# Optimization experiments

Hardware: AMD Instinct MI355X
Metric: run time of the kernel (lower is better)

## Reference

```python
import jax, jax.numpy as jnp
import numpy as np
import math

B, N, D, O, H = 2, 3072, 64, 64, 4

def setup_inputs() -> dict:
    key = jax.random.key(0)
    ks = jax.random.split(key, 8)
    x = jax.random.normal(ks[0], (B, N, D), dtype=jnp.float32)
    edge_index = jax.random.randint(ks[1], (B, N, N), 0, 2, dtype=jnp.int32)
    s = 1.0 / math.sqrt(D)
    Wv = jax.random.uniform(ks[2], (H, D, O), jnp.float32, -s, s)
    bv = jax.random.uniform(ks[3], (H, O), jnp.float32, -s, s)
    Wq = jax.random.uniform(ks[4], (H, D, O), jnp.float32, -s, s)
    bq = jax.random.uniform(ks[5], (H, O), jnp.float32, -s, s)
    Wk = jax.random.uniform(ks[6], (H, D, O), jnp.float32, -s, s)
    bk = jax.random.uniform(ks[7], (H, O), jnp.float32, -s, s)
    return {"x": x, "edge_index": edge_index, "Wv": Wv, "bv": bv,
            "Wq": Wq, "bq": bq, "Wk": Wk, "bk": bk}

def reference(x, edge_index, Wv, bv, Wq, bq, Wk, bk):
    # x: [B,N,D]; edge_index: dense {0,1} adjacency [B,N,N]
    dk = jnp.asarray(math.sqrt(x.shape[-1]), x.dtype)
    v = jnp.einsum('bnd,hdo->bhno', x, Wv) + bv[None, :, None, :]
    q = jnp.einsum('bnd,hdo->bhno', x, Wq) + bq[None, :, None, :]
    k = jnp.einsum('bnd,hdo->bhno', x, Wk) + bk[None, :, None, :]
    scores = jnp.einsum('bhno,bhmo->bhnm', q, k) / dk        # [B,H,N,N]
    scores = jax.nn.leaky_relu(scores, 0.2)
    mask = (-1e10) * (1.0 - edge_index.astype(scores.dtype))  # [B,N,N]
    scores = scores + mask[:, None, :, :]
    prop = jax.nn.softmax(scores, axis=-1)
    # dropout on v omitted (inference mode: identity)
    feats = jnp.einsum('bhnm,bhmo->bhno', prop, v)            # [B,H,N,O]
    out = jnp.mean(feats, axis=1)                             # [B,N,O]
    return jax.nn.leaky_relu(out, 0.2)
```

## Files before the change

### kernel.cpp

```cpp
#include <hip/hip_runtime.h>
#include <hip/hip_bf16.h>
#include <cstdint>

#define Bc 2
#define Nc 3072
#define Hc 4
#define NW32 96
#define TILEB 8192

typedef __bf16    bf16x8 __attribute__((ext_vector_type(8)));
typedef _Float16  f16x8  __attribute__((ext_vector_type(8)));
typedef float     f32x16 __attribute__((ext_vector_type(16)));

#define QSCALE 0.18033688f

static __device__ __forceinline__ f32x16 mfma32bf(bf16x8 a, bf16x8 b, f32x16 c) {
    return __builtin_amdgcn_mfma_f32_32x32x16_bf16(a, b, c, 0, 0, 0);
}
static __device__ __forceinline__ f32x16 mfma32h(f16x8 a, f16x8 b, f32x16 c) {
    return __builtin_amdgcn_mfma_f32_32x32x16_f16(a, b, c, 0, 0, 0);
}
static __device__ __forceinline__ void gload_lds16(const void* g, void* l) {
    __builtin_amdgcn_global_load_lds((const __attribute__((address_space(1))) void*)g,
                                     (__attribute__((address_space(3))) void*)l, 16, 0, 0);
}
static __device__ __forceinline__ uint32_t pkrtz(float lo, float hi) {
    uint32_t w;
    asm("v_cvt_pkrtz_f16_f32 %0, %1, %2" : "=v"(w) : "v"(lo), "v"(hi));
    return w;
}

static __device__ __forceinline__ void softmax_pack(const f32x16& sc, uint32_t mwh,
                                                    uint32_t W8[8], float& lsum)
{
    #pragma unroll
    for (int i = 0; i < 8; ++i) {
        const int bp0 = (2*i & 3) + 8*(2*i >> 2);
        float s0 = sc[2*i], s1 = sc[2*i + 1];
        float a0 = fmaxf(s0, 0.2f*s0);
        float a1 = fmaxf(s1, 0.2f*s1);
        float e0, e1;
        asm("v_exp_f32 %0, %1" : "=v"(e0) : "v"(a0));
        asm("v_exp_f32 %0, %1" : "=v"(e1) : "v"(a1));
        uint32_t m0 = (uint32_t)(((int)(mwh << (31 - bp0))) >> 31);
        uint32_t m1 = (uint32_t)(((int)(mwh << (30 - bp0))) >> 31);
        float p0 = __uint_as_float(__float_as_uint(e0) & m0);
        float p1 = __uint_as_float(__float_as_uint(e1) & m1);
        lsum += p0 + p1;
        W8[i] = pkrtz(p0, p1);
    }
}

static __device__ __forceinline__ void assemble_pa(uint32_t W8[8], f16x8& pa0, f16x8& pa1)
{
    uint32_t a0 = W8[0], a2 = W8[2], a1 = W8[1], a3 = W8[3];
    uint32_t b0 = W8[4], b2 = W8[6], b1 = W8[5], b3 = W8[7];
    asm("v_permlane32_swap_b32 %0, %1" : "+v"(a0), "+v"(a2));
    asm("v_permlane32_swap_b32 %0, %1" : "+v"(a1), "+v"(a3));
    asm("v_permlane32_swap_b32 %0, %1" : "+v"(b0), "+v"(b2));
    asm("v_permlane32_swap_b32 %0, %1" : "+v"(b1), "+v"(b3));
    union { uint32_t u[4]; f16x8 v; } u0, u1;
    u0.u[0] = a0; u0.u[1] = a1; u0.u[2] = a2; u0.u[3] = a3;
    u1.u[0] = b0; u1.u[1] = b1; u1.u[2] = b2; u1.u[3] = b3;
    pa0 = u0.v; pa1 = u1.v;
}

__global__ void prep_kernel(const float* __restrict__ Wq, const float* __restrict__ Wk,
                            const float* __restrict__ Wv,
                            const float* __restrict__ bq, const float* __restrict__ bk,
                            const float* __restrict__ bv, const float* __restrict__ x,
                            __bf16* __restrict__ Wbh, __bf16* __restrict__ Wbl,
                            float* __restrict__ Bs,
                            __bf16* __restrict__ Xh, __bf16* __restrict__ Xl)
{
    if (blockIdx.x < 192) {
        int i = blockIdx.x*256 + threadIdx.x;
        int d = i & 63, o = (i >> 6) & 63, h = (i >> 12) & 3, p = i >> 14;
        const float* W = (p == 0) ? Wq : (p == 1) ? Wk : Wv;
        float scale = (p == 0) ? QSCALE : 1.0f;
        float val = W[(h*64 + d)*64 + o] * scale;
        int idx = (((p*Hc + h)*64 + o) << 6) + d;
        __bf16 hi = (__bf16)val;
        Wbh[idx] = hi;
        Wbl[idx] = (__bf16)(val - (float)hi);
        if (i < 3*Hc*64) {
            int pp = i / (Hc*64), rest = i % (Hc*64);
            const float* B = (pp == 0) ? bq : (pp == 1) ? bk : bv;
            Bs[i] = B[rest] * ((pp == 0) ? QSCALE : 1.0f);
        }
    } else {
        int i = (blockIdx.x - 192)*256 + threadIdx.x;
        const float4* xp = (const float4*)(x + (size_t)i*8);
        float4 a = xp[0], c = xp[1];
        float v[8] = {a.x, a.y, a.z, a.w, c.x, c.y, c.z, c.w};
        bf16x8 h, l;
        #pragma unroll
        for (int j = 0; j < 8; ++j) {
            __bf16 hh = (__bf16)v[j];
            h[j] = hh;
            l[j] = (__bf16)(v[j] - (float)hh);
        }
        *(bf16x8*)(Xh + (size_t)i*8) = h;
        *(bf16x8*)(Xl + (size_t)i*8) = l;
    }
}

__global__ __launch_bounds__(256) void qkv_mfma(
    const __bf16* __restrict__ Xh, const __bf16* __restrict__ Xl,
    const __bf16* __restrict__ Wbh, const __bf16* __restrict__ Wbl,
    const float* __restrict__ Bs,
    _Float16* __restrict__ Qf, _Float16* __restrict__ Kf,
    _Float16* __restrict__ KVimg)
{
    const int lane = threadIdx.x & 63, w = threadIdx.x >> 6;
    const int l31 = lane & 31, hi = lane >> 5;
    int t = blockIdx.x;
    int nt = t % 48; t /= 48;
    int b  = t & 1;  t >>= 1;
    int p  = t % 3;
    int h  = t / 3;
    const int r0 = (w >> 1)*32, c0 = (w & 1)*32, n0 = nt*64;

    bf16x8 xh[4], xl[4], wh[4], wl[4];
    #pragma unroll
    for (int kk = 0; kk < 4; ++kk) {
        size_t xoff = (((size_t)(b*Nc + n0 + r0 + l31)) << 6) + kk*16 + hi*8;
        xh[kk] = *(const bf16x8*)(Xh + xoff);
        xl[kk] = *(const bf16x8*)(Xl + xoff);
        size_t woff = (((size_t)((p*Hc + h)*64 + c0 + l31)) << 6) + kk*16 + hi*8;
        wh[kk] = *(const bf16x8*)(Wbh + woff);
        wl[kk] = *(const bf16x8*)(Wbl + woff);
    }
    float bias = Bs[(p*Hc + h)*64 + c0 + l31];
    f32x16 acc;
    #pragma unroll
    for (int i = 0; i < 16; ++i) acc[i] = bias;
    #pragma unroll
    for (int kk = 0; kk < 4; ++kk) {
        acc = mfma32bf(xh[kk], wh[kk], acc);
        acc = mfma32bf(xl[kk], wh[kk], acc);
        acc = mfma32bf(xh[kk], wl[kk], acc);
    }
    const int bh = b*Hc + h;
    if (p < 2) {
        _Float16* dst = (p == 0) ? Qf : Kf;
        #pragma unroll
        for (int r = 0; r < 16; ++r) {
            int row = (r & 3) + 8*(r >> 2) + 4*hi;
            size_t idx = (((size_t)bh*Nc + n0 + r0 + row) << 6) + c0 + l31;
            dst[idx] = (_Float16)acc[r];
        }
    } else {
        const int t_img = (n0 + r0) >> 5;
        char* img = (char*)KVimg + (size_t)(bh*96 + t_img)*TILEB;
        #pragma unroll
        for (int grp = 0; grp < 2; ++grp) {
            uint32_t wH[4];
            #pragma unroll
            for (int j = 0; j < 4; ++j)
                wH[j] = pkrtz(acc[grp*8 + 2*j], acc[grp*8 + 2*j + 1]);
            asm("v_permlane32_swap_b32 %0, %1" : "+v"(wH[0]), "+v"(wH[2]));
            asm("v_permlane32_swap_b32 %0, %1" : "+v"(wH[1]), "+v"(wH[3]));
            const int kb = grp*2 + hi;
            const int o  = c0 + l31;
            uint4 gh = {wH[0], wH[1], wH[2], wH[3]};
            *(uint4*)(img + 4096 + ((kb*64 + o) << 4)) = gh;
        }
    }
}

__global__ void imgk_kernel(const _Float16* __restrict__ Kf, _Float16* __restrict__ KVimg)
{
    const int t = blockIdx.x % 96, bh = blockIdx.x / 96;
    char* img = (char*)KVimg + (size_t)(bh*96 + t)*TILEB;
    int dc = threadIdx.x & 7, key = threadIdx.x >> 3;
    size_t src = (((size_t)bh*Nc + t*32 + key) << 6) + dc*8;
    *(uint4*)(img + (dc*32 + key)*16) = *(const uint4*)(Kf + src);
}

__global__ void pack_kernel(const int* __restrict__ edge, uint32_t* __restrict__ pmT)
{
    int gw = blockIdx.x*4 + (threadIdx.x >> 6);
    int lane = threadIdx.x & 63;
    int ng = gw % 48; gw /= 48;
    int w  = gw % NW32; gw /= NW32;
    int b  = gw;
    int n = ng*64 + lane;
    const uint4* ep = (const uint4*)(edge + ((size_t)b*Nc + n)*Nc + w*32);
    uint32_t word = 0;
    #pragma unroll
    for (int i = 0; i < 8; ++i) {
        uint4 e = ep[i];
        word |= (e.x ? 1u : 0u) << (4*i);
        word |= (e.y ? 1u : 0u) << (4*i + 1);
        word |= (e.z ? 1u : 0u) << (4*i + 2);
        word |= (e.w ? 1u : 0u) << (4*i + 3);
    }
    pmT[((size_t)b*NW32 + w)*Nc + n] = word;
}

__global__ __launch_bounds__(256, 3) void attn_mfma(
    const _Float16* __restrict__ Qf,
    const _Float16* __restrict__ KVimg, const uint32_t* __restrict__ pmT,
    float* __restrict__ PA, float* __restrict__ PL, int KS, int tps)
{
    __shared__ __align__(16) char lds[3][2*TILEB];
    const int lane = threadIdx.x & 63, w = threadIdx.x >> 6;
    const int l31 = lane & 31, hi = lane >> 5;
    int gb = blockIdx.x;
    const int bh = gb & 7; gb >>= 3;
    const int qt = gb % 24;
    const int ks = gb / 24;
    const int b = bh >> 2;
    const int qrow0 = qt*128 + w*32;
    const int t0 = ks*tps;
    const int iters = tps >> 1;

    const uint32_t* pmp = pmT + ((size_t)b*NW32 + t0)*Nc + qrow0 + l31;
    uint32_t mw0 = pmp[0];
    uint32_t mw1 = pmp[Nc];
    __builtin_amdgcn_sched_barrier(0);
    const char* gsrc = (const char*)KVimg + (size_t)(bh*96 + t0)*TILEB
                     + w*4096 + lane*16;
    #pragma unroll
    for (int g = 0; g < 4; ++g)
        gload_lds16(gsrc + g*1024, &lds[0][w*4096 + g*1024]);

    f16x8 qf[4];
    #pragma unroll
    for (int kk = 0; kk < 4; ++kk) {
        size_t qoff = (((size_t)bh*Nc + qrow0 + l31) << 6) + kk*16 + hi*8;
        qf[kk] = *(const f16x8*)(Qf + qoff);
    }

    f32x16 acc0, acc1;
    #pragma unroll
    for (int i = 0; i < 16; ++i) { acc0[i] = 0.f; acc1[i] = 0.f; }
    float lsum = 0.f;

    char *bA = &lds[0][0], *bB = &lds[1][0], *bC = &lds[2][0];
    #pragma unroll 1
    for (int it = 0; it < iters; ++it) {
        const int adv = (it + 1 < iters) ? 1 : 0;
        const size_t moff = (size_t)(adv ? 2 : 0) * Nc;
        uint32_t nmw0 = pmp[moff];
        uint32_t nmw1 = pmp[moff + Nc];
        pmp += moff;
        __builtin_amdgcn_sched_barrier(0);
        const char* gnext = gsrc + (adv ? 2*TILEB : 0);
        {
            char* ldst = bB + w*4096;
            #pragma unroll
            for (int g = 0; g < 4; ++g)
                gload_lds16(gnext + g*1024, ldst + g*1024);
        }
        gsrc = gnext;
        asm volatile("s_waitcnt vmcnt(6)" ::: "memory");
        __builtin_amdgcn_s_barrier();

        f32x16 sc0, sc1;
        #pragma unroll
        for (int i = 0; i < 16; ++i) { sc0[i] = 0.f; sc1[i] = 0.f; }
        __builtin_amdgcn_s_setprio(1);
        #pragma unroll
        for (int kk = 0; kk < 4; ++kk) {
            f16x8 k0 = *(const f16x8*)(bA + ((kk*2 + hi) << 9) + (l31 << 4));
            f16x8 k1 = *(const f16x8*)(bA + TILEB + ((kk*2 + hi) << 9) + (l31 << 4));
            sc0 = mfma32h(k0, qf[kk], sc0);
            sc1 = mfma32h(k1, qf[kk], sc1);
        }
        __builtin_amdgcn_s_setprio(0);

        uint32_t W80[8], W81[8];
        softmax_pack(sc0, mw0 >> (hi*4), W80, lsum);
        softmax_pack(sc1, mw1 >> (hi*4), W81, lsum);
        mw0 = nmw0; mw1 = nmw1;
        f16x8 pa00, pa01, pa10, pa11;
        assemble_pa(W80, pa00, pa01);
        assemble_pa(W81, pa10, pa11);

        __builtin_amdgcn_s_setprio(1);
        #pragma unroll
        for (int u = 0; u < 2; ++u) {
            #pragma unroll
            for (int kkp = 0; kkp < 2; ++kkp) {
                f16x8 pa = u ? (kkp ? pa11 : pa10) : (kkp ? pa01 : pa00);
                #pragma unroll
                for (int ot = 0; ot < 2; ++ot) {
                    f16x8 vh = *(const f16x8*)(bA + u*TILEB + 4096
                                               + ((kkp*2 + hi) << 10)
                                               + ((ot*32 + l31) << 4));
                    if (ot == 0) acc0 = mfma32h(pa, vh, acc0);
                    else         acc1 = mfma32h(pa, vh, acc1);
                }
            }
        }
        __builtin_amdgcn_s_setprio(0);

        char* tmp = bA; bA = bB; bB = bC; bC = tmp;
    }

    float* po = PA + (((size_t)(bh*KS + ks)*Nc + qrow0) << 6);
    #pragma unroll
    for (int r = 0; r < 16; ++r) {
        int row = (r & 3) + 8*(r >> 2) + 4*hi;
        po[((size_t)row << 6) + l31]      = acc0[r];
        po[((size_t)row << 6) + 32 + l31] = acc1[r];
    }
    lsum += __shfl_xor(lsum, 32);
    if (lane < 32)
        PL[(size_t)(bh*KS + ks)*Nc + qrow0 + l31] = lsum;
}

__global__ void merge_kernel(const float* __restrict__ PA, const float* __restrict__ PL,
                             float* __restrict__ out, int KS)
{
    int gid = blockIdx.x*256 + threadIdx.x;
    int o  = gid & 63;
    int bn = gid >> 6;
    int n  = bn % Nc;
    int b  = bn / Nc;
    float ft = 0.f;
    for (int h = 0; h < Hc; ++h) {
        int bh = b*Hc + h;
        float A = 0.f, L = 0.f;
        for (int ks = 0; ks < KS; ++ks) {
            A += PA[(((size_t)(bh*KS + ks)*Nc + n) << 6) + o];
            L += PL[(size_t)(bh*KS + ks)*Nc + n];
        }
        ft += A / L;
    }
    ft *= 0.25f;
    out[((size_t)bn << 6) + o] = fmaxf(ft, 0.f) + 0.2f*fminf(ft, 0.f);
}

extern "C" void kernel_launch(void* const* d_in, const int* in_sizes, int n_in,
                              void* d_out, int out_size, void* d_ws, size_t ws_size,
                              hipStream_t stream)
{
    const float* x    = (const float*)d_in[0];
    const int*   edge = (const int*)d_in[1];
    const float* Wv   = (const float*)d_in[2];
    const float* bv   = (const float*)d_in[3];
    const float* Wq   = (const float*)d_in[4];
    const float* bq   = (const float*)d_in[5];
    const float* Wk   = (const float*)d_in[6];
    const float* bk   = (const float*)d_in[7];
    float* out = (float*)d_out;

    const size_t PROJ = (size_t)Bc*Hc*Nc*64;
    char* p = (char*)d_ws;
    __bf16* Wbh = (__bf16*)p;     p += 49152*2;
    __bf16* Wbl = (__bf16*)p;     p += 49152*2;
    float*  Bs  = (float*)p;      p += 4096;
    __bf16* Xh  = (__bf16*)p;     p += (size_t)Bc*Nc*64*2;
    __bf16* Xl  = (__bf16*)p;     p += (size_t)Bc*Nc*64*2;
    _Float16* Qf = (_Float16*)p;  p += PROJ*2;
    _Float16* Kf = (_Float16*)p;  p += PROJ*2;
    _Float16* KVimg = (_Float16*)p; p += (size_t)Bc*Hc*96*TILEB;
    uint32_t* pmT = (uint32_t*)p; p += (size_t)Bc*NW32*Nc*4;

    int KS = 4;
    for (;;) {
        size_t need = (size_t)(p - (char*)d_ws)
                    + (size_t)Bc*Hc*KS*Nc*64*4 + (size_t)Bc*Hc*KS*Nc*4;
        if (need <= ws_size || KS == 1) break;
        KS >>= 1;
    }
    float* PA = (float*)p;        p += (size_t)Bc*Hc*KS*Nc*64*4;
    float* PL = (float*)p;

    hipLaunchKernelGGL(prep_kernel, dim3(384),  dim3(256), 0, stream,
                       Wq, Wk, Wv, bq, bk, bv, x, Wbh, Wbl, Bs, Xh, Xl);
    hipLaunchKernelGGL(qkv_mfma,    dim3(1152), dim3(256), 0, stream,
                       Xh, Xl, Wbh, Wbl, Bs, Qf, Kf, KVimg);
    hipLaunchKernelGGL(imgk_kernel, dim3(Bc*Hc*96), dim3(256), 0, stream, Kf, KVimg);
    hipLaunchKernelGGL(pack_kernel, dim3(Bc*NW32*48/4), dim3(256), 0, stream, edge, pmT);
    hipLaunchKernelGGL(attn_mfma,   dim3(8*KS*24), dim3(256), 0, stream,
                       Qf, KVimg, pmT, PA, PL, KS, 96/KS);
    hipLaunchKernelGGL(merge_kernel, dim3((Bc*Nc*64)/256), dim3(256), 0, stream,
                       PA, PL, out, KS);
}
```

Baseline: 80.93 us.

## Split attention K tiles across wave pairs, MFMA row sums, fuse x split into qkv

The attention kernel now runs 512 threads per block. Two waves share each 32-row query slab and take alternating K tiles, and their partial accumulators are combined through LDS at the end. The softmax denominator is now computed by an MFMA against a ones vector instead of scalar adds, and masking is applied to the packed f16 values. The bf16 hi/lo split of x moves from the prep kernel into qkv_mfma, which drops the Xh/Xl workspace round trip, and the split count is fixed at compile time. Risks include register pressure under the (512,6) launch bounds, the extra LDS reduction, and a small precision change in the row sum.

```diff
diff --git a/kernel.cpp b/kernel.cpp
--- a/kernel.cpp
+++ b/kernel.cpp
@@ -7,6 +7,8 @@
 #define Hc 4
 #define NW32 96
 #define TILEB 8192
+#define KSC 4
+#define TPS (NW32/KSC)
 
 typedef __bf16    bf16x8 __attribute__((ext_vector_type(8)));
 typedef _Float16  f16x8  __attribute__((ext_vector_type(8)));
@@ -31,7 +33,7 @@
 }
 
 static __device__ __forceinline__ void softmax_pack(const f32x16& sc, uint32_t mwh,
-                                                    uint32_t W8[8], float& lsum)
+                                                    uint32_t W8[8])
 {
     #pragma unroll
     for (int i = 0; i < 8; ++i) {
@@ -42,12 +44,10 @@
         float e0, e1;
         asm("v_exp_f32 %0, %1" : "=v"(e0) : "v"(a0));
         asm("v_exp_f32 %0, %1" : "=v"(e1) : "v"(a1));
+        uint32_t pk = pkrtz(e0, e1);
         uint32_t m0 = (uint32_t)(((int)(mwh << (31 - bp0))) >> 31);
         uint32_t m1 = (uint32_t)(((int)(mwh << (30 - bp0))) >> 31);
-        float p0 = __uint_as_float(__float_as_uint(e0) & m0);
-        float p1 = __uint_as_float(__float_as_uint(e1) & m1);
-        lsum += p0 + p1;
-        W8[i] = pkrtz(p0, p1);
+        W8[i] = pk & ((m0 & 0x0000ffffu) | (m1 & 0xffff0000u));
     }
 }
 
@@ -68,45 +68,28 @@
 __global__ void prep_kernel(const float* __restrict__ Wq, const float* __restrict__ Wk,
                             const float* __restrict__ Wv,
                             const float* __restrict__ bq, const float* __restrict__ bk,
-                            const float* __restrict__ bv, const float* __restrict__ x,
+                            const float* __restrict__ bv,
                             __bf16* __restrict__ Wbh, __bf16* __restrict__ Wbl,
-                            float* __restrict__ Bs,
-                            __bf16* __restrict__ Xh, __bf16* __restrict__ Xl)
-{
-    if (blockIdx.x < 192) {
-        int i = blockIdx.x*256 + threadIdx.x;
-        int d = i & 63, o = (i >> 6) & 63, h = (i >> 12) & 3, p = i >> 14;
-        const float* W = (p == 0) ? Wq : (p == 1) ? Wk : Wv;
-        float scale = (p == 0) ? QSCALE : 1.0f;
-        float val = W[(h*64 + d)*64 + o] * scale;
-        int idx = (((p*Hc + h)*64 + o) << 6) + d;
-        __bf16 hi = (__bf16)val;
-        Wbh[idx] = hi;
-        Wbl[idx] = (__bf16)(val - (float)hi);
-        if (i < 3*Hc*64) {
-            int pp = i / (Hc*64), rest = i % (Hc*64);
-            const float* B = (pp == 0) ? bq : (pp == 1) ? bk : bv;
-            Bs[i] = B[rest] * ((pp == 0) ? QSCALE : 1.0f);
-        }
-    } else {
-        int i = (blockIdx.x - 192)*256 + threadIdx.x;
-        const float4* xp = (const float4*)(x + (size_t)i*8);
-        float4 a = xp[0], c = xp[1];
-        float v[8] = {a.x, a.y, a.z, a.w, c.x, c.y, c.z, c.w};
-        bf16x8 h, l;
-        #pragma unroll
-        for (int j = 0; j < 8; ++j) {
-            __bf16 hh = (__bf16)v[j];
-            h[j] = hh;
-            l[j] = (__bf16)(v[j] - (float)hh);
-        }
-        *(bf16x8*)(Xh + (size_t)i*8) = h;
-        *(bf16x8*)(Xl + (size_t)i*8) = l;
+                            float* __restrict__ Bs)
+{
+    int i = blockIdx.x*256 + threadIdx.x;
+    int d = i & 63, o = (i >> 6) & 63, h = (i >> 12) & 3, p = i >> 14;
+    const float* W = (p == 0) ? Wq : (p == 1) ? Wk : Wv;
+    float scale = (p == 0) ? QSCALE : 1.0f;
+    float val = W[(h*64 + d)*64 + o] * scale;
+    int idx = (((p*Hc + h)*64 + o) << 6) + d;
+    __bf16 hi = (__bf16)val;
+    Wbh[idx] = hi;
+    Wbl[idx] = (__bf16)(val - (float)hi);
+    if (i < 3*Hc*64) {
+        int pp = i / (Hc*64), rest = i % (Hc*64);
+        const float* B = (pp == 0) ? bq : (pp == 1) ? bk : bv;
+        Bs[i] = B[rest] * ((pp == 0) ? QSCALE : 1.0f);
     }
 }
 
 __global__ __launch_bounds__(256) void qkv_mfma(
-    const __bf16* __restrict__ Xh, const __bf16* __restrict__ Xl,
+    const float* __restrict__ x,
     const __bf16* __restrict__ Wbh, const __bf16* __restrict__ Wbl,
     const float* __restrict__ Bs,
     _Float16* __restrict__ Qf, _Float16* __restrict__ Kf,
@@ -125,8 +108,15 @@
     #pragma unroll
     for (int kk = 0; kk < 4; ++kk) {
         size_t xoff = (((size_t)(b*Nc + n0 + r0 + l31)) << 6) + kk*16 + hi*8;
-        xh[kk] = *(const bf16x8*)(Xh + xoff);
-        xl[kk] = *(const bf16x8*)(Xl + xoff);
+        float4 f0 = *(const float4*)(x + xoff);
+        float4 f1 = *(const float4*)(x + xoff + 4);
+        float xs[8] = {f0.x, f0.y, f0.z, f0.w, f1.x, f1.y, f1.z, f1.w};
+        #pragma unroll
+        for (int j = 0; j < 8; ++j) {
+            __bf16 hh = (__bf16)xs[j];
+            xh[kk][j] = hh;
+            xl[kk][j] = (__bf16)(xs[j] - (float)hh);
+        }
         size_t woff = (((size_t)((p*Hc + h)*64 + c0 + l31)) << 6) + kk*16 + hi*8;
         wh[kk] = *(const bf16x8*)(Wbh + woff);
         wl[kk] = *(const bf16x8*)(Wbl + woff);
@@ -199,32 +189,32 @@
     pmT[((size_t)b*NW32 + w)*Nc + n] = word;
 }
 
-__global__ __launch_bounds__(256, 3) void attn_mfma(
+__global__ __launch_bounds__(512, 6) void attn_mfma(
     const _Float16* __restrict__ Qf,
     const _Float16* __restrict__ KVimg, const uint32_t* __restrict__ pmT,
-    float* __restrict__ PA, float* __restrict__ PL, int KS, int tps)
+    float* __restrict__ PA, float* __restrict__ PL)
 {
     __shared__ __align__(16) char lds[3][2*TILEB];
     const int lane = threadIdx.x & 63, w = threadIdx.x >> 6;
     const int l31 = lane & 31, hi = lane >> 5;
+    const int p2 = w >> 1;
+    const int u  = w & 1;
     int gb = blockIdx.x;
     const int bh = gb & 7; gb >>= 3;
     const int qt = gb % 24;
     const int ks = gb / 24;
-    const int b = bh >> 2;
-    const int qrow0 = qt*128 + w*32;
-    const int t0 = ks*tps;
-    const int iters = tps >> 1;
-
-    const uint32_t* pmp = pmT + ((size_t)b*NW32 + t0)*Nc + qrow0 + l31;
-    uint32_t mw0 = pmp[0];
-    uint32_t mw1 = pmp[Nc];
+    const int b = gb >= 0 ? (bh >> 2) : 0;
+    const int qrow0 = qt*128 + p2*32;
+    const int t0 = ks*TPS;
+
+    const uint32_t* pmp = pmT + ((size_t)b*NW32 + t0 + u)*Nc + qrow0 + l31;
+    uint32_t mw_cur = pmp[0];
     __builtin_amdgcn_sched_barrier(0);
-    const char* gsrc = (const char*)KVimg + (size_t)(bh*96 + t0)*TILEB
-                     + w*4096 + lane*16;
-    #pragma unroll
-    for (int g = 0; g < 4; ++g)
-        gload_lds16(gsrc + g*1024, &lds[0][w*4096 + g*1024]);
+    const char* gbase = (const char*)KVimg + (size_t)(bh*96 + t0)*TILEB
+                      + w*2048 + lane*16;
+    #pragma unroll
+    for (int g = 0; g < 2; ++g)
+        gload_lds16(gbase + g*1024, &lds[0][w*2048 + g*1024]);
 
     f16x8 qf[4];
     #pragma unroll
@@ -232,88 +222,111 @@
         size_t qoff = (((size_t)bh*Nc + qrow0 + l31) << 6) + kk*16 + hi*8;
         qf[kk] = *(const f16x8*)(Qf + qoff);
     }
-
-    f32x16 acc0, acc1;
-    #pragma unroll
-    for (int i = 0; i < 16; ++i) { acc0[i] = 0.f; acc1[i] = 0.f; }
-    float lsum = 0.f;
-
-    char *bA = &lds[0][0], *bB = &lds[1][0], *bC = &lds[2][0];
+    f16x8 ones;
+    #pragma unroll
+    for (int j = 0; j < 8; ++j) ones[j] = (_Float16)1.0f;
+    f32x16 fzero;
+    #pragma unroll
+    for (int i = 0; i < 16; ++i) fzero[i] = 0.f;
+
+    f32x16 acc0 = fzero, acc1 = fzero, acc2 = fzero;
+
     #pragma unroll 1
-    for (int it = 0; it < iters; ++it) {
-        const int adv = (it + 1 < iters) ? 1 : 0;
-        const size_t moff = (size_t)(adv ? 2 : 0) * Nc;
-        uint32_t nmw0 = pmp[moff];
-        uint32_t nmw1 = pmp[moff + Nc];
-        pmp += moff;
-        __builtin_amdgcn_sched_barrier(0);
-        const char* gnext = gsrc + (adv ? 2*TILEB : 0);
-        {
-            char* ldst = bB + w*4096;
+    for (int s = 0; s < 4; ++s) {
+        #pragma unroll
+        for (int j = 0; j < 3; ++j) {
+            uint32_t mw_next = pmp[(size_t)(j + 1)*2*Nc];
+            __builtin_amdgcn_sched_barrier(0);
+            {
+                char* ldst = &lds[(j + 1) % 3][w*2048];
+                const char* gs = gbase + (size_t)(j + 1)*2*TILEB;
+                #pragma unroll
+                for (int g = 0; g < 2; ++g)
+                    gload_lds16(gs + g*1024, ldst + g*1024);
+            }
+            asm volatile("s_waitcnt vmcnt(3)" ::: "memory");
+            __builtin_amdgcn_s_barrier();
+            asm volatile("" ::: "memory");
+            const char* Lb = &lds[j][u*TILEB];
+
+            f32x16 sc;
+            __builtin_amdgcn_s_setprio(1);
+            {
+                f16x8 k0 = *(const f16x8*)(Lb + (hi << 9) + (l31 << 4));
+                sc = mfma32h(k0, qf[0], fzero);
+            }
             #pragma unroll
-            for (int g = 0; g < 4; ++g)
-                gload_lds16(gnext + g*1024, ldst + g*1024);
-        }
-        gsrc = gnext;
-        asm volatile("s_waitcnt vmcnt(6)" ::: "memory");
-        __builtin_amdgcn_s_barrier();
-
-        f32x16 sc0, sc1;
-        #pragma unroll
-        for (int i = 0; i < 16; ++i) { sc0[i] = 0.f; sc1[i] = 0.f; }
-        __builtin_amdgcn_s_setprio(1);
-        #pragma unroll
-        for (int kk = 0; kk < 4; ++kk) {
-            f16x8 k0 = *(const f16x8*)(bA + ((kk*2 + hi) << 9) + (l31 << 4));
-            f16x8 k1 = *(const f16x8*)(bA + TILEB + ((kk*2 + hi) << 9) + (l31 << 4));
-            sc0 = mfma32h(k0, qf[kk], sc0);
-            sc1 = mfma32h(k1, qf[kk], sc1);
-        }
-        __builtin_amdgcn_s_setprio(0);
-
-        uint32_t W80[8], W81[8];
-        softmax_pack(sc0, mw0 >> (hi*4), W80, lsum);
-        softmax_pack(sc1, mw1 >> (hi*4), W81, lsum);
-        mw0 = nmw0; mw1 = nmw1;
-        f16x8 pa00, pa01, pa10, pa11;
-        assemble_pa(W80, pa00, pa01);
-        assemble_pa(W81, pa10, pa11);
-
-        __builtin_amdgcn_s_setprio(1);
-        #pragma unroll
-        for (int u = 0; u < 2; ++u) {
+            for (int kk = 1; kk < 4; ++kk) {
+                f16x8 k0 = *(const f16x8*)(Lb + ((kk*2 + hi) << 9) + (l31 << 4));
+                sc = mfma32h(k0, qf[kk], sc);
+            }
+            __builtin_amdgcn_s_setprio(0);
+
+            uint32_t W8[8];
+            softmax_pack(sc, mw_cur >> (hi*4), W8);
+            mw_cur = mw_next;
+            f16x8 pa0, pa1;
+            assemble_pa(W8, pa0, pa1);
+
+            __builtin_amdgcn_s_setprio(1);
+            acc2 = mfma32h(pa0, ones, acc2);
+            acc2 = mfma32h(pa1, ones, acc2);
             #pragma unroll
             for (int kkp = 0; kkp < 2; ++kkp) {
-                f16x8 pa = u ? (kkp ? pa11 : pa10) : (kkp ? pa01 : pa00);
+                f16x8 pa = kkp ? pa1 : pa0;
                 #pragma unroll
                 for (int ot = 0; ot < 2; ++ot) {
-                    f16x8 vh = *(const f16x8*)(bA + u*TILEB + 4096
-                                               + ((kkp*2 + hi) << 10)
+                    f16x8 vh = *(const f16x8*)(Lb + 4096 + ((kkp*2 + hi) << 10)
                                                + ((ot*32 + l31) << 4));
                     if (ot == 0) acc0 = mfma32h(pa, vh, acc0);
                     else         acc1 = mfma32h(pa, vh, acc1);
                 }
             }
-        }
-        __builtin_amdgcn_s_setprio(0);
-
-        char* tmp = bA; bA = bB; bB = bC; bC = tmp;
-    }
-
-    float* po = PA + (((size_t)(bh*KS + ks)*Nc + qrow0) << 6);
-    #pragma unroll
-    for (int r = 0; r < 16; ++r) {
-        int row = (r & 3) + 8*(r >> 2) + 4*hi;
-        po[((size_t)row << 6) + l31]      = acc0[r];
-        po[((size_t)row << 6) + 32 + l31] = acc1[r];
-    }
-    lsum += __shfl_xor(lsum, 32);
-    if (lane < 32)
-        PL[(size_t)(bh*KS + ks)*Nc + qrow0 + l31] = lsum;
+            __builtin_amdgcn_s_setprio(0);
+            asm volatile("" ::: "memory");
+        }
+        pmp   += (size_t)6*Nc;
+        gbase += (size_t)6*TILEB;
+    }
+
+    asm volatile("s_waitcnt vmcnt(0)" ::: "memory");
+    __syncthreads();
+
+    float* xb = (float*)&lds[0][0];
+    if (u) {
+        #pragma unroll
+        for (int r = 0; r < 16; ++r) {
+            xb[(r)      *256 + p2*64 + lane] = acc0[r];
+            xb[(16 + r) *256 + p2*64 + lane] = acc1[r];
+            xb[(32 + r) *256 + p2*64 + lane] = acc2[r];
+        }
+    }
+    __syncthreads();
+    if (!u) {
+        #pragma unroll
+        for (int r = 0; r < 16; ++r) {
+            acc0[r] += xb[(r)      *256 + p2*64 + lane];
+            acc1[r] += xb[(16 + r) *256 + p2*64 + lane];
+            acc2[r] += xb[(32 + r) *256 + p2*64 + lane];
+        }
+        float* po = PA + (((size_t)(bh*KSC + ks)*Nc + qrow0) << 6);
+        #pragma unroll
+        for (int r = 0; r < 16; ++r) {
+            int row = (r & 3) + 8*(r >> 2) + 4*hi;
+            po[((size_t)row << 6) + l31]      = acc0[r];
+            po[((size_t)row << 6) + 32 + l31] = acc1[r];
+        }
+        if (l31 == 0) {
+            float* pl = PL + (size_t)(bh*KSC + ks)*Nc + qrow0;
+            #pragma unroll
+            for (int r = 0; r < 16; ++r)
+                pl[(r & 3) + 8*(r >> 2) + 4*hi] = acc2[r];
+        }
+    }
 }
 
 __global__ void merge_kernel(const float* __restrict__ PA, const float* __restrict__ PL,
-                             float* __restrict__ out, int KS)
+                             float* __restrict__ out)
 {
     int gid = blockIdx.x*256 + threadIdx.x;
     int o  = gid & 63;
@@ -324,9 +337,9 @@
     for (int h = 0; h < Hc; ++h) {
         int bh = b*Hc + h;
         float A = 0.f, L = 0.f;
-        for (int ks = 0; ks < KS; ++ks) {
-            A += PA[(((size_t)(bh*KS + ks)*Nc + n) << 6) + o];
-            L += PL[(size_t)(bh*KS + ks)*Nc + n];
+        for (int ks = 0; ks < KSC; ++ks) {
+            A += PA[(((size_t)(bh*KSC + ks)*Nc + n) << 6) + o];
+            L += PL[(size_t)(bh*KSC + ks)*Nc + n];
         }
         ft += A / L;
     }
@@ -353,31 +366,21 @@
     __bf16* Wbh = (__bf16*)p;     p += 49152*2;
     __bf16* Wbl = (__bf16*)p;     p += 49152*2;
     float*  Bs  = (float*)p;      p += 4096;
-    __bf16* Xh  = (__bf16*)p;     p += (size_t)Bc*Nc*64*2;
-    __bf16* Xl  = (__bf16*)p;     p += (size_t)Bc*Nc*64*2;
     _Float16* Qf = (_Float16*)p;  p += PROJ*2;
     _Float16* Kf = (_Float16*)p;  p += PROJ*2;
     _Float16* KVimg = (_Float16*)p; p += (size_t)Bc*Hc*96*TILEB;
     uint32_t* pmT = (uint32_t*)p; p += (size_t)Bc*NW32*Nc*4;
-
-    int KS = 4;
-    for (;;) {
-        size_t need = (size_t)(p - (char*)d_ws)
-                    + (size_t)Bc*Hc*KS*Nc*64*4 + (size_t)Bc*Hc*KS*Nc*4;
-        if (need <= ws_size || KS == 1) break;
-        KS >>= 1;
-    }
-    float* PA = (float*)p;        p += (size_t)Bc*Hc*KS*Nc*64*4;
+    float* PA = (float*)p;        p += (size_t)Bc*Hc*KSC*Nc*64*4;
     float* PL = (float*)p;
 
-    hipLaunchKernelGGL(prep_kernel, dim3(384),  dim3(256), 0, stream,
-                       Wq, Wk, Wv, bq, bk, bv, x, Wbh, Wbl, Bs, Xh, Xl);
+    hipLaunchKernelGGL(prep_kernel, dim3(192),  dim3(256), 0, stream,
+                       Wq, Wk, Wv, bq, bk, bv, Wbh, Wbl, Bs);
     hipLaunchKernelGGL(qkv_mfma,    dim3(1152), dim3(256), 0, stream,
-                       Xh, Xl, Wbh, Wbl, Bs, Qf, Kf, KVimg);
+                       x, Wbh, Wbl, Bs, Qf, Kf, KVimg);
     hipLaunchKernelGGL(imgk_kernel, dim3(Bc*Hc*96), dim3(256), 0, stream, Kf, KVimg);
     hipLaunchKernelGGL(pack_kernel, dim3(Bc*NW32*48/4), dim3(256), 0, stream, edge, pmT);
-    hipLaunchKernelGGL(attn_mfma,   dim3(8*KS*24), dim3(256), 0, stream,
-                       Qf, KVimg, pmT, PA, PL, KS, 96/KS);
+    hipLaunchKernelGGL(attn_mfma,   dim3(8*KSC*24), dim3(512), 0, stream,
+                       Qf, KVimg, pmT, PA, PL);
     hipLaunchKernelGGL(merge_kernel, dim3((Bc*Nc*64)/256), dim3(256), 0, stream,
-                       PA, PL, out, KS);
-}
+                       PA, PL, out);
+}
```

Result: slower. 132.7 us (+63.9%).
